# Kernel optimization log

Measured on AMD Instinct MI355X. Metric: run time of the kernel, lower is better.

Reference implementation:

```python
import jax, jax.numpy as jnp
import numpy as np

N0, N1, N2, N3 = 262144, 65536, 16384, 4096
EPS = 1e-5  # BatchNorm1d default eps


def setup_inputs() -> dict:
    key = jax.random.key(0)
    ks = jax.random.split(key, 10)
    f0 = jax.random.normal(ks[0], (N0, 64), dtype=jnp.float32)
    f1 = jax.random.normal(ks[1], (N1, 128), dtype=jnp.float32)
    f2 = jax.random.normal(ks[2], (N2, 256), dtype=jnp.float32)
    f3 = jax.random.normal(ks[3], (N3, 512), dtype=jnp.float32)
    # upsampling indices: finer level gathers from coarser level
    idx0 = jax.random.randint(ks[4], (N2,), 0, N3, dtype=jnp.int32)   # f3 -> level2
    idx1 = jax.random.randint(ks[5], (N1,), 0, N2, dtype=jnp.int32)   # f2 -> level1
    idx2 = jax.random.randint(ks[6], (N0,), 0, N1, dtype=jnp.int32)   # f1 -> level0
    # BN weight init'd to constant 0.25 in the module; bias defaults to 0
    bn_w2, bn_b2 = jnp.full((512,), 0.25, jnp.float32), jnp.zeros((512,), jnp.float32)
    bn_w1, bn_b1 = jnp.full((256,), 0.25, jnp.float32), jnp.zeros((256,), jnp.float32)
    bn_w0, bn_b0 = jnp.full((128,), 0.25, jnp.float32), jnp.zeros((128,), jnp.float32)
    # Linear(in, out, bias=False) weights, torch layout [out, in]
    W2 = jax.random.normal(ks[7], (256, 512), dtype=jnp.float32) * 0.02
    W1 = jax.random.normal(ks[8], (128, 256), dtype=jnp.float32) * 0.02
    W0 = jax.random.normal(ks[9], (64, 128), dtype=jnp.float32) * 0.02
    return dict(f0=f0, f1=f1, f2=f2, f3=f3,
                bn_w2=bn_w2, bn_b2=bn_b2, W2=W2,
                bn_w1=bn_w1, bn_b1=bn_b1, W1=W1,
                bn_w0=bn_w0, bn_b0=bn_b0, W0=W0,
                idx0=idx0, idx1=idx1, idx2=idx2)


def _decode(f, bn_w, bn_b, W):
    # BatchNorm1d (training-mode batch stats, biased variance) -> Linear (no bias)
    mean = jnp.mean(f, axis=0)
    var = jnp.var(f, axis=0)
    xn = (f - mean) * jax.lax.rsqrt(var + EPS)
    return (xn * bn_w + bn_b) @ W.T  # [N, out_ch]


def reference(f0, f1, f2, f3, bn_w2, bn_b2, W2, bn_w1, bn_b1, W1,
              bn_w0, bn_b0, W0, idx0, idx1, idx2):
    # gather (upsample) -> BN -> Linear -> residual add, coarse to fine
    f2 = f2 + _decode(f3[idx0], bn_w2, bn_b2, W2)   # [N2, 256]
    f1 = f1 + _decode(f2[idx1], bn_w1, bn_b1, W1)   # [N1, 128]
    f0 = f0 + _decode(f1[idx2], bn_w0, bn_b0, W0)   # [N0, 64]
    return f0
```

## Files before the change

kernel.cpp:

```cpp
#include <hip/hip_runtime.h>

#define BN_EPS 1e-5f

constexpr int PN0 = 262144, PN1 = 65536, PN2 = 16384, PN3 = 4096;
constexpr size_t MB = 1u << 20;

typedef __attribute__((ext_vector_type(8))) short short8;
typedef __attribute__((ext_vector_type(4))) float f32x4;
typedef __attribute__((ext_vector_type(4))) unsigned int u32x4;

__device__ __forceinline__ unsigned f2bf(float f) {
    unsigned u = __builtin_bit_cast(unsigned, f);
    u += 0x7fff + ((u >> 16) & 1);
    return u >> 16;
}
__device__ __forceinline__ float bf2f(unsigned h) {
    return __builtin_bit_cast(float, h << 16);
}
__device__ __forceinline__ f32x4 ntload4(const float* p) {
    return __builtin_nontemporal_load(reinterpret_cast<const f32x4*>(p));
}
__device__ __forceinline__ void ntstore4(float* p, f32x4 v) {
    __builtin_nontemporal_store(v, reinterpret_cast<f32x4*>(p));
}
#define SCHED_FENCE() __builtin_amdgcn_sched_barrier(0)

struct MegaArgs {
    const float *f0, *f1, *f2, *f3;
    const float *bnw2, *bnb2, *W2;
    const float *bnw1, *bnb1, *W1;
    const float *bnw0, *bnb0, *W0;
    const int *idx0, *idx1, *idx2;
    unsigned short *f3bf, *dec2, *dec1, *dec0, *f2p, *f1p;
    int *cnt2, *cnt1;
    float *part2, *part1, *part0;
    float *out;
};

template<int G, int NL>
__device__ __forceinline__ void red_write(float* aux, const float s[8], const float q[8],
                                          int t, int lr, int cgi,
                                          float* part, int vb, int C) {
    #pragma unroll
    for (int j = 0; j < 8; ++j) aux[(lr * G + cgi) * 8 + j] = s[j];
    __syncthreads();
    if (t < G) {
        float ss[8] = {};
        for (int l = 0; l < NL; ++l)
            #pragma unroll
            for (int j = 0; j < 8; ++j) ss[j] += aux[(l * G + t) * 8 + j];
        #pragma unroll
        for (int j = 0; j < 8; ++j)
            part[((size_t)vb * C + t * 8 + j) * 2] = ss[j];
    }
    __syncthreads();
    #pragma unroll
    for (int j = 0; j < 8; ++j) aux[(lr * G + cgi) * 8 + j] = q[j];
    __syncthreads();
    if (t < G) {
        float qq[8] = {};
        for (int l = 0; l < NL; ++l)
            #pragma unroll
            for (int j = 0; j < 8; ++j) qq[j] += aux[(l * G + t) * 8 + j];
        #pragma unroll
        for (int j = 0; j < 8; ++j)
            part[((size_t)vb * C + t * 8 + j) * 2 + 1] = qq[j];
    }
}

__global__ __launch_bounds__(256) void k_p1(MegaArgs a) {
    __shared__ float aux[2048];
    const int vb = blockIdx.x;
    const int t = threadIdx.x;
    if (vb < 128) {
        const int cgi = t & 63, lr = t >> 6;
        const int r0 = vb * 128;
        float s[8] = {}, q[8] = {};
        for (int ii = 0; ii < 4; ++ii) {
            int gi[8];
            #pragma unroll
            for (int j = 0; j < 8; ++j) gi[j] = a.idx0[r0 + lr + 4 * (ii * 8 + j)];
            float4 x0[8], x1[8];
            #pragma unroll
            for (int j = 0; j < 8; ++j) {
                const float* p = a.f3 + (size_t)gi[j] * 512 + cgi * 8;
                x0[j] = *reinterpret_cast<const float4*>(p);
                x1[j] = *reinterpret_cast<const float4*>(p + 4);
            }
            SCHED_FENCE();
            #pragma unroll
            for (int j = 0; j < 8; ++j) {
                float v[8] = {x0[j].x, x0[j].y, x0[j].z, x0[j].w,
                              x1[j].x, x1[j].y, x1[j].z, x1[j].w};
                #pragma unroll
                for (int k = 0; k < 8; ++k) { s[k] += v[k]; q[k] += v[k] * v[k]; }
            }
        }
        red_write<64, 4>(aux, s, q, t, lr, cgi, a.part2, vb, 512);
    } else if (vb < 256) {
        const int cgi = t & 63, lr = t >> 6;
        const int r0 = (vb - 128) * 32;
        float4 x0[8], x1[8];
        #pragma unroll
        for (int i = 0; i < 8; ++i) {
            const float* p = a.f3 + (size_t)(r0 + lr + 4 * i) * 512 + cgi * 8;
            x0[i] = *reinterpret_cast<const float4*>(p);
            x1[i] = *reinterpret_cast<const float4*>(p + 4);
        }
        SCHED_FENCE();
        #pragma unroll
        for (int i = 0; i < 8; ++i) {
            uint4 o;
            o.x = f2bf(x0[i].x) | (f2bf(x0[i].y) << 16);
            o.y = f2bf(x0[i].z) | (f2bf(x0[i].w) << 16);
            o.z = f2bf(x1[i].x) | (f2bf(x1[i].y) << 16);
            o.w = f2bf(x1[i].z) | (f2bf(x1[i].w) << 16);
            *reinterpret_cast<uint4*>(a.f3bf + (size_t)(r0 + lr + 4 * i) * 512 + cgi * 8) = o;
        }
    } else if (vb < 288) {
        int b = vb - 256;
        int v[8];
        #pragma unroll
        for (int i = 0; i < 8; ++i) v[i] = a.idx1[b * 2048 + i * 256 + t];
        SCHED_FENCE();
        #pragma unroll
        for (int i = 0; i < 8; ++i) atomicAdd(&a.cnt2[v[i]], 1);
    } else {
        int b = vb - 288;
        int v[8];
        #pragma unroll
        for (int i = 0; i < 8; ++i) v[i] = a.idx2[b * 2048 + i * 256 + t];
        SCHED_FENCE();
        #pragma unroll
        for (int i = 0; i < 8; ++i) atomicAdd(&a.cnt1[v[i]], 1);
    }
}

template<int K, int NB, int NT>
__device__ void calc_scsh(int tid, const float* part, const float* bnw, const float* bnb,
                          float invN, float* sc, float* sh) {
    for (int c = tid; c < K; c += NT) {
        float s = 0.f, q = 0.f;
        for (int b = 0; b < NB; ++b) {
            float2 p = *reinterpret_cast<const float2*>(part + ((size_t)b * K + c) * 2);
            s += p.x;
            q += p.y;
        }
        float mean = s * invN;
        float var = fmaxf(q * invN - mean * mean, 0.f);
        float scl = bnw[c] * rsqrtf(var + BN_EPS);
        sc[c] = scl;
        sh[c] = bnb[c] - mean * scl;
    }
    __syncthreads();
}

__global__ __launch_bounds__(512) void k_g2(MegaArgs a) {
    constexpr int K = 512;
    __shared__ __align__(16) unsigned short Wl[32 * 512];
    __shared__ float scshB[1088];
    float* sc = scshB;
    float* sh = scshB + 512;
    float* dl = scshB + 1024;
    const int tid = threadIdx.x;
    calc_scsh<512, 128, 512>(tid, a.part2, a.bnw2, a.bnb2, 1.f / PN2, sc, sh);
    const int lane = tid & 63;
    const int w = tid >> 6;
    const int l15 = lane & 15, lg = lane >> 4;
    const int n32 = tid >> 4, kc = tid & 15;

    const int vb = blockIdx.x;
    const int chunk = vb & 31, panel = vb >> 5;
    const int row = chunk * 128 + w * 16 + l15;
    const unsigned short* xp = a.f3bf + (size_t)row * K + lg * 8;
    short8 xf[16];
    #pragma unroll
    for (int kk = 0; kk < 16; ++kk)
        xf[kk] = *reinterpret_cast<const short8*>(xp + kk * 32);

    {
        const float* wrow = a.W2 + (size_t)(panel * 32 + n32) * K;
        float dp = 0.f;
        #pragma unroll
        for (int i = 0; i < 4; ++i) {
            int k = kc * 32 + i * 8;
            float4 w0 = *reinterpret_cast<const float4*>(wrow + k);
            float4 w1 = *reinterpret_cast<const float4*>(wrow + k + 4);
            float4 s0 = *reinterpret_cast<const float4*>(&sc[k]);
            float4 s1 = *reinterpret_cast<const float4*>(&sc[k + 4]);
            float4 h0 = *reinterpret_cast<const float4*>(&sh[k]);
            float4 h1 = *reinterpret_cast<const float4*>(&sh[k + 4]);
            dp += h0.x * w0.x + h0.y * w0.y + h0.z * w0.z + h0.w * w0.w
                + h1.x * w1.x + h1.y * w1.y + h1.z * w1.z + h1.w * w1.w;
            uint4 o;
            o.x = f2bf(w0.x * s0.x) | (f2bf(w0.y * s0.y) << 16);
            o.y = f2bf(w0.z * s0.z) | (f2bf(w0.w * s0.w) << 16);
            o.z = f2bf(w1.x * s1.x) | (f2bf(w1.y * s1.y) << 16);
            o.w = f2bf(w1.z * s1.z) | (f2bf(w1.w * s1.w) << 16);
            int si = (n32 * K + k) ^ ((n32 & 7) << 3);
            *reinterpret_cast<uint4*>(&Wl[si]) = o;
        }
        dp += __shfl_xor(dp, 1); dp += __shfl_xor(dp, 2);
        dp += __shfl_xor(dp, 4); dp += __shfl_xor(dp, 8);
        if (kc == 0) dl[n32] = dp;
    }
    __syncthreads();

    f32x4 acc[2];
    acc[0] = (f32x4){0.f, 0.f, 0.f, 0.f};
    acc[1] = (f32x4){0.f, 0.f, 0.f, 0.f};
    #pragma unroll
    for (int kk = 0; kk < 16; ++kk) {
        #pragma unroll
        for (int ni = 0; ni < 2; ++ni) {
            const int si = ((ni * 16 + l15) * K + kk * 32 + lg * 8) ^ ((l15 & 7) << 3);
            short8 wf = *reinterpret_cast<const short8*>(&Wl[si]);
            acc[ni] = __builtin_amdgcn_mfma_f32_16x16x32_bf16(wf, xf[kk], acc[ni], 0, 0, 0);
        }
    }

    const size_t rowoff = (size_t)row * 256 + panel * 32;
    #pragma unroll
    for (int ni = 0; ni < 2; ++ni) {
        float4 dr = *reinterpret_cast<const float4*>(&dl[ni * 16 + lg * 4]);
        size_t off = rowoff + ni * 16 + lg * 4;
        float v0 = dr.x + acc[ni][0];
        float v1 = dr.y + acc[ni][1];
        float v2 = dr.z + acc[ni][2];
        float v3 = dr.w + acc[ni][3];
        *reinterpret_cast<uint2*>(&a.dec2[off]) =
            make_uint2(f2bf(v0) | (f2bf(v1) << 16), f2bf(v2) | (f2bf(v3) << 16));
    }
}

__global__ __launch_bounds__(512) void k_g1(MegaArgs a) {
    constexpr int K = 256;
    __shared__ __align__(16) unsigned short Wl[64 * 256];
    __shared__ float scshB[576];
    float* sc = scshB;
    float* sh = scshB + 256;
    float* dl = scshB + 512;
    const int tid = threadIdx.x;
    calc_scsh<256, 256, 512>(tid, a.part1, a.bnw1, a.bnb1, 1.f / PN1, sc, sh);
    const int lane = tid & 63;
    const int w = tid >> 6;
    const int l15 = lane & 15, lg = lane >> 4;
    const int n = tid >> 3, kc = tid & 7;

    const int vb = blockIdx.x;
    const int chunk = vb & 127, panel = vb >> 7;
    const int row = chunk * 128 + w * 16 + l15;
    const unsigned short* xp = a.f2p + (size_t)row * K + lg * 8;
    short8 xf[8];
    #pragma unroll
    for (int kk = 0; kk < 8; ++kk)
        xf[kk] = *reinterpret_cast<const short8*>(xp + kk * 32);

    {
        const float* wrow = a.W1 + (size_t)(panel * 64 + n) * K;
        float dp = 0.f;
        #pragma unroll
        for (int i = 0; i < 4; ++i) {
            int k = kc * 32 + i * 8;
            float4 w0 = *reinterpret_cast<const float4*>(wrow + k);
            float4 w1 = *reinterpret_cast<const float4*>(wrow + k + 4);
            float4 s0 = *reinterpret_cast<const float4*>(&sc[k]);
            float4 s1 = *reinterpret_cast<const float4*>(&sc[k + 4]);
            float4 h0 = *reinterpret_cast<const float4*>(&sh[k]);
            float4 h1 = *reinterpret_cast<const float4*>(&sh[k + 4]);
            dp += h0.x * w0.x + h0.y * w0.y + h0.z * w0.z + h0.w * w0.w
                + h1.x * w1.x + h1.y * w1.y + h1.z * w1.z + h1.w * w1.w;
            uint4 o;
            o.x = f2bf(w0.x * s0.x) | (f2bf(w0.y * s0.y) << 16);
            o.y = f2bf(w0.z * s0.z) | (f2bf(w0.w * s0.w) << 16);
            o.z = f2bf(w1.x * s1.x) | (f2bf(w1.y * s1.y) << 16);
            o.w = f2bf(w1.z * s1.z) | (f2bf(w1.w * s1.w) << 16);
            int si = (n * K + k) ^ ((n & 7) << 3);
            *reinterpret_cast<uint4*>(&Wl[si]) = o;
        }
        dp += __shfl_xor(dp, 1); dp += __shfl_xor(dp, 2); dp += __shfl_xor(dp, 4);
        if (kc == 0) dl[n] = dp;
    }
    __syncthreads();

    f32x4 acc[4];
    #pragma unroll
    for (int ni = 0; ni < 4; ++ni) acc[ni] = (f32x4){0.f, 0.f, 0.f, 0.f};
    #pragma unroll
    for (int kk = 0; kk < 8; ++kk) {
        #pragma unroll
        for (int ni = 0; ni < 4; ++ni) {
            const int si = ((ni * 16 + l15) * K + kk * 32 + lg * 8) ^ ((l15 & 7) << 3);
            short8 wf = *reinterpret_cast<const short8*>(&Wl[si]);
            acc[ni] = __builtin_amdgcn_mfma_f32_16x16x32_bf16(wf, xf[kk], acc[ni], 0, 0, 0);
        }
    }

    const size_t rowoff = (size_t)row * 128 + panel * 64;
    #pragma unroll
    for (int ni = 0; ni < 4; ++ni) {
        float4 dr = *reinterpret_cast<const float4*>(&dl[ni * 16 + lg * 4]);
        size_t off = rowoff + ni * 16 + lg * 4;
        float v0 = dr.x + acc[ni][0];
        float v1 = dr.y + acc[ni][1];
        float v2 = dr.z + acc[ni][2];
        float v3 = dr.w + acc[ni][3];
        *reinterpret_cast<uint2*>(&a.dec1[off]) =
            make_uint2(f2bf(v0) | (f2bf(v1) << 16), f2bf(v2) | (f2bf(v3) << 16));
    }
}

__global__ __launch_bounds__(512) void k_g0(MegaArgs a) {
    constexpr int K = 128;
    __shared__ __align__(16) unsigned short Wl[64 * 128];
    __shared__ float scshB[320];
    float* sc = scshB;
    float* sh = scshB + 128;
    float* dl = scshB + 256;
    const int tid = threadIdx.x;
    calc_scsh<128, 512, 512>(tid, a.part0, a.bnw0, a.bnb0, 1.f / PN0, sc, sh);
    const int lane = tid & 63;
    const int w = tid >> 6;
    const int l15 = lane & 15, lg = lane >> 4;
    const int n = tid >> 3, kc = tid & 7;

    {
        const float* wrow = a.W0 + (size_t)n * K;
        float dp = 0.f;
        #pragma unroll
        for (int i = 0; i < 2; ++i) {
            int k = kc * 16 + i * 8;
            float4 w0 = *reinterpret_cast<const float4*>(wrow + k);
            float4 w1 = *reinterpret_cast<const float4*>(wrow + k + 4);
            float4 s0 = *reinterpret_cast<const float4*>(&sc[k]);
            float4 s1 = *reinterpret_cast<const float4*>(&sc[k + 4]);
            float4 h0 = *reinterpret_cast<const float4*>(&sh[k]);
            float4 h1 = *reinterpret_cast<const float4*>(&sh[k + 4]);
            dp += h0.x * w0.x + h0.y * w0.y + h0.z * w0.z + h0.w * w0.w
                + h1.x * w1.x + h1.y * w1.y + h1.z * w1.z + h1.w * w1.w;
            uint4 o;
            o.x = f2bf(w0.x * s0.x) | (f2bf(w0.y * s0.y) << 16);
            o.y = f2bf(w0.z * s0.z) | (f2bf(w0.w * s0.w) << 16);
            o.z = f2bf(w1.x * s1.x) | (f2bf(w1.y * s1.y) << 16);
            o.w = f2bf(w1.z * s1.z) | (f2bf(w1.w * s1.w) << 16);
            int si = (n * K + k) ^ ((n & 7) << 3);
            *reinterpret_cast<uint4*>(&Wl[si]) = o;
        }
        dp += __shfl_xor(dp, 1); dp += __shfl_xor(dp, 2); dp += __shfl_xor(dp, 4);
        if (kc == 0) dl[n] = dp;
    }
    __syncthreads();

    float4 dr[4];
    #pragma unroll
    for (int ni = 0; ni < 4; ++ni)
        dr[ni] = *reinterpret_cast<const float4*>(&dl[ni * 16 + lg * 4]);

    const int vb = blockIdx.x;
    const int row = vb * 128 + w * 16 + l15;
    const unsigned short* xp = a.f1p + (size_t)row * K + lg * 8;
    short8 xf[4];
    #pragma unroll
    for (int kk = 0; kk < 4; ++kk)
        xf[kk] = *reinterpret_cast<const short8*>(xp + kk * 32);
    f32x4 acc[4];
    #pragma unroll
    for (int ni = 0; ni < 4; ++ni) acc[ni] = (f32x4){0.f, 0.f, 0.f, 0.f};
    #pragma unroll
    for (int kk = 0; kk < 4; ++kk) {
        #pragma unroll
        for (int ni = 0; ni < 4; ++ni) {
            const int si = ((ni * 16 + l15) * K + kk * 32 + lg * 8) ^ ((l15 & 7) << 3);
            short8 wf = *reinterpret_cast<const short8*>(&Wl[si]);
            acc[ni] = __builtin_amdgcn_mfma_f32_16x16x32_bf16(wf, xf[kk], acc[ni], 0, 0, 0);
        }
    }
    const size_t rowoff = (size_t)row * 64;
    #pragma unroll
    for (int ni = 0; ni < 4; ++ni) {
        size_t off = rowoff + ni * 16 + lg * 4;
        float v0 = dr[ni].x + acc[ni][0];
        float v1 = dr[ni].y + acc[ni][1];
        float v2 = dr[ni].z + acc[ni][2];
        float v3 = dr[ni].w + acc[ni][3];
        *reinterpret_cast<uint2*>(&a.dec0[off]) =
            make_uint2(f2bf(v0) | (f2bf(v1) << 16), f2bf(v2) | (f2bf(v3) << 16));
    }
}

template<int C, int IT, bool STATS, bool OUT_F32>
__device__ void ga_body(int vb, int t, const float* base,
                        const unsigned short* dec, const int* idx,
                        const int* cnt_next, void* outv, float* part,
                        float* aux) {
    constexpr int G = C / 8;
    constexpr int NL = 256 / G;
    const int cgi = t % G;
    const int lr = t / G;
    const int r0 = vb * (NL * IT);

    int g[IT];
    #pragma unroll
    for (int i = 0; i < IT; ++i) g[i] = idx[r0 + lr + NL * i];

    float wreg[IT];
    if constexpr (STATS) {
        #pragma unroll
        for (int i = 0; i < IT; ++i) wreg[i] = (float)cnt_next[r0 + lr + NL * i];
    }

    u32x4 dv[IT];
    #pragma unroll
    for (int i = 0; i < IT; ++i)
        dv[i] = *reinterpret_cast<const u32x4*>(dec + (size_t)g[i] * C + cgi * 8);

    f32x4 b0[IT], b1[IT];
    #pragma unroll
    for (int i = 0; i < IT; ++i) {
        const float* bp = base + (size_t)(r0 + lr + NL * i) * C + cgi * 8;
        b0[i] = ntload4(bp);
        b1[i] = ntload4(bp + 4);
    }

    SCHED_FENCE();

    float s[8] = {}, q[8] = {};
    #pragma unroll
    for (int i = 0; i < IT; ++i) {
        const int r = r0 + lr + NL * i;
        float v[8];
        v[0] = b0[i][0] + bf2f(dv[i][0] & 0xffffu);
        v[1] = b0[i][1] + bf2f(dv[i][0] >> 16);
        v[2] = b0[i][2] + bf2f(dv[i][1] & 0xffffu);
        v[3] = b0[i][3] + bf2f(dv[i][1] >> 16);
        v[4] = b1[i][0] + bf2f(dv[i][2] & 0xffffu);
        v[5] = b1[i][1] + bf2f(dv[i][2] >> 16);
        v[6] = b1[i][2] + bf2f(dv[i][3] & 0xffffu);
        v[7] = b1[i][3] + bf2f(dv[i][3] >> 16);
        if constexpr (OUT_F32) {
            float* op = (float*)outv + (size_t)r * C + cgi * 8;
            ntstore4(op, (f32x4){v[0], v[1], v[2], v[3]});
            ntstore4(op + 4, (f32x4){v[4], v[5], v[6], v[7]});
        } else {
            unsigned h[8];
            #pragma unroll
            for (int j = 0; j < 8; ++j) h[j] = f2bf(v[j]);
            u32x4 o = {h[0] | (h[1] << 16), h[2] | (h[3] << 16),
                       h[4] | (h[5] << 16), h[6] | (h[7] << 16)};
            *reinterpret_cast<u32x4*>((unsigned short*)outv + (size_t)r * C + cgi * 8) = o;
            if constexpr (STATS) {
                #pragma unroll
                for (int j = 0; j < 8; ++j) {
                    float rv = bf2f(h[j]);
                    s[j] += wreg[i] * rv;
                    q[j] += wreg[i] * rv * rv;
                }
            }
        }
    }

    if constexpr (STATS)
        red_write<G, NL>(aux, s, q, t, lr, cgi, part, vb, C);
}

__global__ __launch_bounds__(256) void k_a2(MegaArgs a) {
    __shared__ float aux[2048];
    ga_body<256, 8, true, false>(blockIdx.x, threadIdx.x, a.f2, a.dec2, a.idx0, a.cnt2,
                                 a.f2p, a.part1, aux);
}
__global__ __launch_bounds__(256) void k_a1(MegaArgs a) {
    __shared__ float aux[2048];
    ga_body<128, 8, true, false>(blockIdx.x, threadIdx.x, a.f1, a.dec1, a.idx1, a.cnt1,
                                 a.f1p, a.part0, aux);
}
__global__ __launch_bounds__(256) void k_a0(MegaArgs a) {
    ga_body<64, 8, false, true>(blockIdx.x, threadIdx.x, a.f0, a.dec0, a.idx2, nullptr,
                                a.out, nullptr, nullptr);
}

extern "C" void kernel_launch(void* const* d_in, const int* in_sizes, int n_in,
                              void* d_out, int out_size, void* d_ws, size_t ws_size,
                              hipStream_t stream) {
    char* wsb = (char*)d_ws;
    unsigned short* f3bf = (unsigned short*)wsb;
    unsigned short* dec2 = (unsigned short*)(wsb + 4 * MB);
    unsigned short* dec1 = (unsigned short*)(wsb + 6 * MB);
    unsigned short* dec0 = (unsigned short*)(wsb + 10 * MB);
    unsigned short* f2p  = (unsigned short*)(wsb + 18 * MB);
    unsigned short* f1p  = (unsigned short*)(wsb + 26 * MB);
    int* cnt2 = (int*)(wsb + 42 * MB);
    int* cnt1 = cnt2 + PN2;
    float* part2 = (float*)(cnt1 + PN1);
    float* part1 = part2 + 128 * 512 * 2;
    float* part0 = part1 + 256 * 256 * 2;

    MegaArgs a;
    a.f0 = (const float*)d_in[0];
    a.f1 = (const float*)d_in[1];
    a.f2 = (const float*)d_in[2];
    a.f3 = (const float*)d_in[3];
    a.bnw2 = (const float*)d_in[4];
    a.bnb2 = (const float*)d_in[5];
    a.W2 = (const float*)d_in[6];
    a.bnw1 = (const float*)d_in[7];
    a.bnb1 = (const float*)d_in[8];
    a.W1 = (const float*)d_in[9];
    a.bnw0 = (const float*)d_in[10];
    a.bnb0 = (const float*)d_in[11];
    a.W0 = (const float*)d_in[12];
    a.idx0 = (const int*)d_in[13];
    a.idx1 = (const int*)d_in[14];
    a.idx2 = (const int*)d_in[15];
    a.f3bf = f3bf; a.dec2 = dec2; a.dec1 = dec1; a.dec0 = dec0;
    a.f2p = f2p; a.f1p = f1p;
    a.cnt2 = cnt2; a.cnt1 = cnt1;
    a.part2 = part2; a.part1 = part1; a.part0 = part0;
    a.out = (float*)d_out;

    hipMemsetAsync(cnt2, 0, (size_t)(PN2 + PN1) * sizeof(int), stream);

    k_p1<<<416, 256, 0, stream>>>(a);
    k_g2<<<256, 512, 0, stream>>>(a);
    k_a2<<<256, 256, 0, stream>>>(a);
    k_g1<<<256, 512, 0, stream>>>(a);
    k_a1<<<512, 256, 0, stream>>>(a);
    k_g0<<<512, 512, 0, stream>>>(a);
    k_a0<<<1024, 256, 0, stream>>>(a);
}
```

Baseline: 137.3 us.

## Compute level-2 BN stats via histogram-weighted sums over f3 rows

Builds a histogram of idx0 in a new small kernel, then computes the batch-norm sums for the gathered level-2 input as count-weighted sums over the 4096 source rows of f3. This replaces the random gather of 16384 rows. The same pass also writes the bf16 copy of f3, so the separate conversion blocks go away and the partial-sum count drops from 128 to 32. The cost is one extra kernel launch that serialises the idx0 histogram ahead of k_p1.

```diff
diff --git a/kernel.cpp b/kernel.cpp
--- a/kernel.cpp
+++ b/kernel.cpp
@@ -32,7 +32,7 @@
     const float *bnw0, *bnb0, *W0;
     const int *idx0, *idx1, *idx2;
     unsigned short *f3bf, *dec2, *dec1, *dec0, *f2p, *f1p;
-    int *cnt2, *cnt1;
+    int *cnt3, *cnt2, *cnt1;
     float *part2, *part1, *part0;
     float *out;
 };
@@ -68,22 +68,33 @@
     }
 }
 
+__global__ __launch_bounds__(256) void k_h(MegaArgs a) {
+    int b = blockIdx.x, t = threadIdx.x;
+    int v[8];
+    #pragma unroll
+    for (int i = 0; i < 8; ++i) v[i] = a.idx0[b * 2048 + i * 256 + t];
+    SCHED_FENCE();
+    #pragma unroll
+    for (int i = 0; i < 8; ++i) atomicAdd(&a.cnt3[v[i]], 1);
+}
+
 __global__ __launch_bounds__(256) void k_p1(MegaArgs a) {
     __shared__ float aux[2048];
     const int vb = blockIdx.x;
     const int t = threadIdx.x;
-    if (vb < 128) {
+    if (vb < 32) {
         const int cgi = t & 63, lr = t >> 6;
         const int r0 = vb * 128;
         float s[8] = {}, q[8] = {};
         for (int ii = 0; ii < 4; ++ii) {
-            int gi[8];
-            #pragma unroll
-            for (int j = 0; j < 8; ++j) gi[j] = a.idx0[r0 + lr + 4 * (ii * 8 + j)];
+            float w[8];
             float4 x0[8], x1[8];
+            int rr[8];
             #pragma unroll
             for (int j = 0; j < 8; ++j) {
-                const float* p = a.f3 + (size_t)gi[j] * 512 + cgi * 8;
+                rr[j] = r0 + lr + 4 * (ii * 8 + j);
+                w[j] = (float)a.cnt3[rr[j]];
+                const float* p = a.f3 + (size_t)rr[j] * 512 + cgi * 8;
                 x0[j] = *reinterpret_cast<const float4*>(p);
                 x1[j] = *reinterpret_cast<const float4*>(p + 4);
             }
@@ -92,33 +103,22 @@
             for (int j = 0; j < 8; ++j) {
                 float v[8] = {x0[j].x, x0[j].y, x0[j].z, x0[j].w,
                               x1[j].x, x1[j].y, x1[j].z, x1[j].w};
+                uint4 o;
+                o.x = f2bf(v[0]) | (f2bf(v[1]) << 16);
+                o.y = f2bf(v[2]) | (f2bf(v[3]) << 16);
+                o.z = f2bf(v[4]) | (f2bf(v[5]) << 16);
+                o.w = f2bf(v[6]) | (f2bf(v[7]) << 16);
+                *reinterpret_cast<uint4*>(a.f3bf + (size_t)rr[j] * 512 + cgi * 8) = o;
                 #pragma unroll
-                for (int k = 0; k < 8; ++k) { s[k] += v[k]; q[k] += v[k] * v[k]; }
+                for (int k = 0; k < 8; ++k) {
+                    s[k] += w[j] * v[k];
+                    q[k] += w[j] * v[k] * v[k];
+                }
             }
         }
         red_write<64, 4>(aux, s, q, t, lr, cgi, a.part2, vb, 512);
-    } else if (vb < 256) {
-        const int cgi = t & 63, lr = t >> 6;
-        const int r0 = (vb - 128) * 32;
-        float4 x0[8], x1[8];
-        #pragma unroll
-        for (int i = 0; i < 8; ++i) {
-            const float* p = a.f3 + (size_t)(r0 + lr + 4 * i) * 512 + cgi * 8;
-            x0[i] = *reinterpret_cast<const float4*>(p);
-            x1[i] = *reinterpret_cast<const float4*>(p + 4);
-        }
-        SCHED_FENCE();
-        #pragma unroll
-        for (int i = 0; i < 8; ++i) {
-            uint4 o;
-            o.x = f2bf(x0[i].x) | (f2bf(x0[i].y) << 16);
-            o.y = f2bf(x0[i].z) | (f2bf(x0[i].w) << 16);
-            o.z = f2bf(x1[i].x) | (f2bf(x1[i].y) << 16);
-            o.w = f2bf(x1[i].z) | (f2bf(x1[i].w) << 16);
-            *reinterpret_cast<uint4*>(a.f3bf + (size_t)(r0 + lr + 4 * i) * 512 + cgi * 8) = o;
-        }
-    } else if (vb < 288) {
-        int b = vb - 256;
+    } else if (vb < 64) {
+        int b = vb - 32;
         int v[8];
         #pragma unroll
         for (int i = 0; i < 8; ++i) v[i] = a.idx1[b * 2048 + i * 256 + t];
@@ -126,7 +126,7 @@
         #pragma unroll
         for (int i = 0; i < 8; ++i) atomicAdd(&a.cnt2[v[i]], 1);
     } else {
-        int b = vb - 288;
+        int b = vb - 64;
         int v[8];
         #pragma unroll
         for (int i = 0; i < 8; ++i) v[i] = a.idx2[b * 2048 + i * 256 + t];
@@ -163,7 +163,7 @@
     float* sh = scshB + 512;
     float* dl = scshB + 1024;
     const int tid = threadIdx.x;
-    calc_scsh<512, 128, 512>(tid, a.part2, a.bnw2, a.bnb2, 1.f / PN2, sc, sh);
+    calc_scsh<512, 32, 512>(tid, a.part2, a.bnw2, a.bnb2, 1.f / PN2, sc, sh);
     const int lane = tid & 63;
     const int w = tid >> 6;
     const int l15 = lane & 15, lg = lane >> 4;
@@ -488,10 +488,11 @@
     unsigned short* dec0 = (unsigned short*)(wsb + 10 * MB);
     unsigned short* f2p  = (unsigned short*)(wsb + 18 * MB);
     unsigned short* f1p  = (unsigned short*)(wsb + 26 * MB);
-    int* cnt2 = (int*)(wsb + 42 * MB);
+    int* cnt3 = (int*)(wsb + 42 * MB);
+    int* cnt2 = cnt3 + PN3;
     int* cnt1 = cnt2 + PN2;
     float* part2 = (float*)(cnt1 + PN1);
-    float* part1 = part2 + 128 * 512 * 2;
+    float* part1 = part2 + 32 * 512 * 2;
     float* part0 = part1 + 256 * 256 * 2;
 
     MegaArgs a;
@@ -513,13 +514,14 @@
     a.idx2 = (const int*)d_in[15];
     a.f3bf = f3bf; a.dec2 = dec2; a.dec1 = dec1; a.dec0 = dec0;
     a.f2p = f2p; a.f1p = f1p;
-    a.cnt2 = cnt2; a.cnt1 = cnt1;
+    a.cnt3 = cnt3; a.cnt2 = cnt2; a.cnt1 = cnt1;
     a.part2 = part2; a.part1 = part1; a.part0 = part0;
     a.out = (float*)d_out;
 
-    hipMemsetAsync(cnt2, 0, (size_t)(PN2 + PN1) * sizeof(int), stream);
-
-    k_p1<<<416, 256, 0, stream>>>(a);
+    hipMemsetAsync(cnt3, 0, (size_t)(PN3 + PN2 + PN1) * sizeof(int), stream);
+
+    k_h<<<8, 256, 0, stream>>>(a);
+    k_p1<<<192, 256, 0, stream>>>(a);
     k_g2<<<256, 512, 0, stream>>>(a);
     k_a2<<<256, 256, 0, stream>>>(a);
     k_g1<<<256, 512, 0, stream>>>(a);
```

New measurement: 135.8 us (median of 2 runs). No clear change (-1.1%).
